# Kernel tuning notes

Measured on AMD Instinct MI355X. Metric: run time of the kernel, lower is better.

## Reference

```python
import jax, jax.numpy as jnp
import numpy as np

B, S, HID = 2, 2048, 2048
NH, NKV, HD = 16, 8, 128
GROUPS = NH // NKV
EPS = 1e-6
SCALING = HD ** -0.5
ROPE_THETA = 1e6


def setup_inputs() -> dict:
    key = jax.random.key(0)
    ks = jax.random.split(key, 8)
    hidden_states = jax.random.normal(ks[0], (B, S, HID), jnp.float32)
    # RoPE tables (Qwen3 style): [B, S, HD]
    pos = jnp.arange(S, dtype=jnp.float32)
    inv_freq = 1.0 / (ROPE_THETA ** (jnp.arange(0, HD, 2, dtype=jnp.float32) / HD))
    ang = pos[:, None] * inv_freq[None, :]            # [S, HD//2]
    emb = jnp.concatenate([ang, ang], axis=-1)        # [S, HD]
    cos = jnp.broadcast_to(jnp.cos(emb)[None], (B, S, HD))
    sin = jnp.broadcast_to(jnp.sin(emb)[None], (B, S, HD))
    # 4D additive causal mask: 0 on/below diagonal, -1e9 above
    causal = jnp.where(jnp.tril(jnp.ones((S, S), bool)), 0.0, -1e9).astype(jnp.float32)
    attention_mask = jnp.broadcast_to(causal[None, None], (B, 1, S, S))
    sc = 0.02
    wq = jax.random.normal(ks[1], (HID, NH * HD), jnp.float32) * sc
    wk = jax.random.normal(ks[2], (HID, NKV * HD), jnp.float32) * sc
    wv = jax.random.normal(ks[3], (HID, NKV * HD), jnp.float32) * sc
    wo = jax.random.normal(ks[4], (NH * HD, HID), jnp.float32) * sc
    q_norm_w = jnp.ones((HD,), jnp.float32)
    k_norm_w = jnp.ones((HD,), jnp.float32)
    return {"hidden_states": hidden_states, "cos": cos, "sin": sin,
            "attention_mask": attention_mask, "wq": wq, "wk": wk, "wv": wv,
            "wo": wo, "q_norm_w": q_norm_w, "k_norm_w": k_norm_w}


def _rmsnorm(x, w, eps=EPS):
    xf = x.astype(jnp.float32)
    var = jnp.mean(xf * xf, axis=-1, keepdims=True)
    return (xf * jax.lax.rsqrt(var + eps)).astype(x.dtype) * w


def _rotate_half(x):
    x1, x2 = x[..., : HD // 2], x[..., HD // 2:]
    return jnp.concatenate([-x2, x1], axis=-1)


def reference(hidden_states, cos, sin, attention_mask, wq, wk, wv, wo, q_norm_w, k_norm_w):
    # projections
    q = jnp.einsum('bsh,hd->bsd', hidden_states, wq).reshape(B, S, NH, HD)
    k = jnp.einsum('bsh,hd->bsd', hidden_states, wk).reshape(B, S, NKV, HD)
    v = jnp.einsum('bsh,hd->bsd', hidden_states, wv).reshape(B, S, NKV, HD)
    # per-head RMSNorm on Q/K (Qwen3RMSNorm over head_dim)
    q = _rmsnorm(q, q_norm_w).transpose(0, 2, 1, 3)   # [B, NH, S, HD]
    k = _rmsnorm(k, k_norm_w).transpose(0, 2, 1, 3)   # [B, NKV, S, HD]
    v = v.transpose(0, 2, 1, 3)                        # [B, NKV, S, HD]
    # RoPE
    c = cos[:, None]  # [B,1,S,HD]
    s = sin[:, None]
    q = q * c + _rotate_half(q) * s
    k = k * c + _rotate_half(k) * s
    # GQA repeat_kv
    k = jnp.repeat(k, GROUPS, axis=1)                  # [B, NH, S, HD]
    v = jnp.repeat(v, GROUPS, axis=1)
    # candidate selection mask: in the source, QK_prune_binary_quant is
    # undefined in this context so the except-branch yields a zero mask -> no-op.
    scores = jnp.einsum('bhqd,bhkd->bhqk', q, k) * SCALING
    scores = scores + attention_mask[:, :, :, :S]      # 4D causal mask branch
    attn_weights = jax.nn.softmax(scores.astype(jnp.float32), axis=-1).astype(q.dtype)
    attn_out = jnp.einsum('bhqk,bhkd->bhqd', attn_weights, v)
    attn_out = attn_out.transpose(0, 2, 1, 3).reshape(B, S, NH * HD)
    attn_out = jnp.einsum('bsd,dh->bsh', attn_out, wo)
    return attn_out, attn_weights
```

## Files before the change

kernel.cpp:

```cpp
#include <hip/hip_runtime.h>
#include <stdint.h>

#define Sn 2048
#define NHn 16
#define NKVn 8
#define HDn 128
#define SCALEf 0.08838834764831845f

using s16x8 = __attribute__((ext_vector_type(8))) short;
using f32x4 = __attribute__((ext_vector_type(4))) float;

__device__ __forceinline__ short f2b(float f) {
  unsigned u = __builtin_bit_cast(unsigned, f);
  u += 0x7fffu + ((u >> 16) & 1u);
  return (short)(u >> 16);
}

__device__ __forceinline__ void gl16(const void* g, void* l) {
  __builtin_amdgcn_global_load_lds((const __attribute__((address_space(1))) void*)g,
                                   (__attribute__((address_space(3))) void*)l, 16, 0, 0);
}

__global__ __launch_bounds__(256) void k_cvt(const float* __restrict__ src, short* __restrict__ dst) {
  int i = blockIdx.x * 256 + threadIdx.x;
  float4 v = ((const float4*)src)[i];
  union { short h[4]; uint2 u; } p;
  p.h[0] = f2b(v.x); p.h[1] = f2b(v.y); p.h[2] = f2b(v.z); p.h[3] = f2b(v.w);
  ((uint2*)dst)[i] = p.u;
}

__global__ __launch_bounds__(256) void k_wt(const float* __restrict__ w, short* __restrict__ wt, int N) {
  __shared__ float t[64][65];
  const int n0 = blockIdx.x * 64, k0 = blockIdx.y * 64;
  const int tid = threadIdx.x;
  const int r = tid >> 2, c0 = (tid & 3) * 16;
  const float* src = w + (size_t)(k0 + r) * N + n0 + c0;
  float4 a = ((const float4*)src)[0];
  float4 b = ((const float4*)src)[1];
  float4 c = ((const float4*)src)[2];
  float4 d = ((const float4*)src)[3];
  float* tr = &t[r][c0];
  tr[0]=a.x; tr[1]=a.y; tr[2]=a.z; tr[3]=a.w;
  tr[4]=b.x; tr[5]=b.y; tr[6]=b.z; tr[7]=b.w;
  tr[8]=c.x; tr[9]=c.y; tr[10]=c.z; tr[11]=c.w;
  tr[12]=d.x; tr[13]=d.y; tr[14]=d.z; tr[15]=d.w;
  __syncthreads();
  union { short h[16]; uint4 u[2]; } p;
#pragma unroll
  for (int j = 0; j < 16; ++j) p.h[j] = f2b(t[c0 + j][r]);
  uint4* dst = (uint4*)(wt + (size_t)(n0 + r) * 2048 + k0 + c0);
  dst[0] = p.u[0]; dst[1] = p.u[1];
}

__global__ __launch_bounds__(256) void k_gemm(const short* __restrict__ A, const short* __restrict__ Bt,
                                              float* __restrict__ C, int M, int N, int K) {
  __shared__ __align__(16) short la[128 * 32];
  __shared__ __align__(16) short lb[128 * 32];
  const int tid = threadIdx.x;
  const int wave = tid >> 6, lane = tid & 63, quad = lane >> 4, lm = lane & 15;
  const int m0 = blockIdx.y * 128, n0 = blockIdx.x * 128;
  const int wm = (wave >> 1) * 64, wn = (wave & 1) * 64;
  const int r0 = tid >> 2, r1 = (256 + tid) >> 2;
  const int q0c = (tid & 3) ^ ((r0 ^ (r0 >> 2)) & 3);
  const int q1c = (tid & 3) ^ ((r1 ^ (r1 >> 2)) & 3);
  const short* gA0 = A + (size_t)(m0 + r0) * K + q0c * 8;
  const short* gA1 = A + (size_t)(m0 + r1) * K + q1c * 8;
  const short* gB0 = Bt + (size_t)(n0 + r0) * K + q0c * 8;
  const short* gB1 = Bt + (size_t)(n0 + r1) * K + q1c * 8;
  short* lA0 = &la[(wave << 6) * 8];
  short* lA1 = &la[(256 + (wave << 6)) * 8];
  short* lB0 = &lb[(wave << 6) * 8];
  short* lB1 = &lb[(256 + (wave << 6)) * 8];
  int aoff[4], boff[4];
#pragma unroll
  for (int mi = 0; mi < 4; ++mi) {
    int r = wm + mi * 16 + lm;
    aoff[mi] = (r * 4 + (quad ^ ((r ^ (r >> 2)) & 3))) * 8;
  }
#pragma unroll
  for (int ni = 0; ni < 4; ++ni) {
    int r = wn + ni * 16 + lm;
    boff[ni] = (r * 4 + (quad ^ ((r ^ (r >> 2)) & 3))) * 8;
  }
  f32x4 acc[4][4] = {};
  for (int k0 = 0; k0 < K; k0 += 32) {
    __syncthreads();
    gl16(gA0 + k0, lA0);
    gl16(gA1 + k0, lA1);
    gl16(gB0 + k0, lB0);
    gl16(gB1 + k0, lB1);
    __syncthreads();
    s16x8 af[4], bfr[4];
#pragma unroll
    for (int mi = 0; mi < 4; ++mi) af[mi] = *(const s16x8*)&la[aoff[mi]];
#pragma unroll
    for (int ni = 0; ni < 4; ++ni) bfr[ni] = *(const s16x8*)&lb[boff[ni]];
#pragma unroll
    for (int mi = 0; mi < 4; ++mi)
#pragma unroll
      for (int ni = 0; ni < 4; ++ni)
        acc[mi][ni] = __builtin_amdgcn_mfma_f32_16x16x32_bf16(af[mi], bfr[ni], acc[mi][ni], 0, 0, 0);
  }
#pragma unroll
  for (int mi = 0; mi < 4; ++mi)
#pragma unroll
    for (int ni = 0; ni < 4; ++ni) {
      size_t base = (size_t)(m0 + wm + mi * 16 + quad * 4) * N + (n0 + wn + ni * 16 + lm);
#pragma unroll
      for (int r = 0; r < 4; ++r)
        C[base + (size_t)r * N] = acc[mi][ni][r];
    }
}

__global__ __launch_bounds__(256) void k_rope(const float* __restrict__ qkv, const float* __restrict__ cosb,
                                              const float* __restrict__ sinb, const float* __restrict__ nw,
                                              short* __restrict__ dst, int nh, int shift, int colbase) {
  const int wid = blockIdx.x * 4 + (threadIdx.x >> 6);
  const int lane = threadIdx.x & 63;
  const int tok = wid >> shift, h = wid & (nh - 1);
  const float* src = qkv + (size_t)tok * 4096 + colbase + h * 128;
  float x0 = src[lane], x1 = src[lane + 64];
  float ss = x0 * x0 + x1 * x1;
#pragma unroll
  for (int off = 32; off > 0; off >>= 1) ss += __shfl_xor(ss, off);
  float rs = rsqrtf(ss * (1.0f / 128.0f) + 1e-6f);
  float xn0 = x0 * rs * nw[lane];
  float xn1 = x1 * rs * nw[lane + 64];
  const float* cb = cosb + (size_t)tok * 128;
  const float* sb = sinb + (size_t)tok * 128;
  float y0 = xn0 * cb[lane] - xn1 * sb[lane];
  float y1 = xn1 * cb[lane + 64] + xn0 * sb[lane + 64];
  int b = tok >> 11, sp = tok & 2047;
  short* d = dst + (((size_t)(b * nh + h)) * 2048 + sp) * 128;
  d[lane] = f2b(y0);
  d[lane + 64] = f2b(y1);
}

__global__ __launch_bounds__(256) void k_vt(const float* __restrict__ qkv, short* __restrict__ VT) {
  __shared__ short t[128 * 66];
  const int tid = threadIdx.x;
  const int s0 = blockIdx.x * 64, hkv = blockIdx.y, b = blockIdx.z;
#pragma unroll
  for (int i = 0; i < 8; ++i) {
    int lin = i * 256 + tid;
    int sl = lin >> 5, d4 = (lin & 31) * 4;
    const float4 v = *(const float4*)(qkv + (size_t)(b * 2048 + s0 + sl) * 4096 + 3072 + hkv * 128 + d4);
    t[(d4 + 0) * 66 + sl] = f2b(v.x);
    t[(d4 + 1) * 66 + sl] = f2b(v.y);
    t[(d4 + 2) * 66 + sl] = f2b(v.z);
    t[(d4 + 3) * 66 + sl] = f2b(v.w);
  }
  __syncthreads();
  const int d = tid >> 1, half = tid & 1;
  union { short h[32]; uint4 u[4]; } p;
#pragma unroll
  for (int j = 0; j < 32; ++j) p.h[j] = t[d * 66 + half * 32 + j];
  uint4* dst = (uint4*)(VT + ((size_t)(b * 8 + hkv) * 128 + d) * 2048 + s0 + half * 32);
  dst[0] = p.u[0]; dst[1] = p.u[1]; dst[2] = p.u[2]; dst[3] = p.u[3];
}

__global__ __launch_bounds__(256) void k_zf(float* __restrict__ W) {
  const int jt = blockIdx.x, it = blockIdx.y, bh = blockIdx.z;
  if (jt <= it) return;
  float* base = W + ((size_t)bh * 2048 + it * 64) * 2048 + jt * 64;
  const float4 z = make_float4(0.f, 0.f, 0.f, 0.f);
#pragma unroll
  for (int i = 0; i < 4; ++i) {
    int lin = i * 256 + threadIdx.x;
    int rr = lin >> 4, c4 = (lin & 15) * 4;
    *(float4*)(base + (size_t)rr * 2048 + c4) = z;
  }
}

__global__ __launch_bounds__(256) void k_attn(const short* __restrict__ Q, const short* __restrict__ Kr,
                                              const short* __restrict__ VT, float* __restrict__ W,
                                              short* __restrict__ OP) {
  __shared__ __align__(16) short qt[64 * 128];
  __shared__ __align__(16) short kt[64 * 128];
  __shared__ __align__(16) short vt[128 * 64];
  __shared__ __align__(16) short pt[64 * 72];
  const int tid = threadIdx.x;
  const int wave = tid >> 6, lane = tid & 63, quad = lane >> 4, lm = lane & 15;
  const int qti = gridDim.x - 1 - blockIdx.x;
  const int h = blockIdx.y, b = blockIdx.z, hkv = h >> 1;
  const int q0 = qti * 64;
  const short* Qb = Q + (((size_t)(b * NHn + h)) * Sn + q0) * HDn;
  const short* Kb = Kr + ((size_t)(b * NKVn + hkv)) * Sn * HDn;
  const short* Vb = VT + ((size_t)(b * NKVn + hkv)) * HDn * Sn;
  float* Wb = W + (((size_t)(b * NHn + h)) * Sn + q0) * (size_t)Sn;

#pragma unroll
  for (int i = 0; i < 4; ++i) {
    int p = i * 256 + tid, r = p >> 4, q = (p & 15) ^ (r & 15);
    gl16(Qb + r * HDn + q * 8, &qt[(i * 256 + (wave << 6)) * 8]);
  }

  float lsum[4] = {0.f, 0.f, 0.f, 0.f};
  for (int jt = 0; jt <= qti; ++jt) {
    const int j0 = jt * 64;
    __syncthreads();
#pragma unroll
    for (int i = 0; i < 4; ++i) {
      int p = i * 256 + tid, r = p >> 4, q = (p & 15) ^ (r & 15);
      gl16(Kb + (size_t)(j0 + r) * HDn + q * 8, &kt[(i * 256 + (wave << 6)) * 8]);
    }
    __syncthreads();
    s16x8 qa[4];
#pragma unroll
    for (int kk = 0; kk < 4; ++kk)
      qa[kk] = *(const s16x8*)&qt[(wave * 16 + lm) * 128 + (((kk * 4 + quad) ^ lm)) * 8];
    f32x4 sa[4] = {};
#pragma unroll
    for (int ni = 0; ni < 4; ++ni)
#pragma unroll
      for (int kk = 0; kk < 4; ++kk) {
        s16x8 kb = *(const s16x8*)&kt[(ni * 16 + lm) * 128 + (((kk * 4 + quad) ^ lm)) * 8];
        sa[ni] = __builtin_amdgcn_mfma_f32_16x16x32_bf16(qa[kk], kb, sa[ni], 0, 0, 0);
      }
    const bool diag = (jt == qti);
#pragma unroll
    for (int ni = 0; ni < 4; ++ni)
#pragma unroll
      for (int r = 0; r < 4; ++r) {
        float e = __expf(sa[ni][r] * SCALEf);
        if (diag && (ni * 16 + lm > wave * 16 + quad * 4 + r)) e = 0.f;
        lsum[r] += e;
      }
  }
  float invl[4];
#pragma unroll
  for (int r = 0; r < 4; ++r) {
    float v = lsum[r];
    v += __shfl_xor(v, 1); v += __shfl_xor(v, 2); v += __shfl_xor(v, 4); v += __shfl_xor(v, 8);
    invl[r] = 1.0f / v;
  }

  f32x4 oa[8] = {};
  for (int jt = 0; jt <= qti; ++jt) {
    const int j0 = jt * 64;
    __syncthreads();
#pragma unroll
    for (int i = 0; i < 4; ++i) {
      int p = i * 256 + tid, r = p >> 4, q = (p & 15) ^ (r & 15);
      gl16(Kb + (size_t)(j0 + r) * HDn + q * 8, &kt[(i * 256 + (wave << 6)) * 8]);
    }
#pragma unroll
    for (int i = 0; i < 4; ++i) {
      int p = i * 256 + tid, r = p >> 3, q = (p & 7) ^ (r & 7);
      gl16(Vb + (size_t)r * Sn + j0 + q * 8, &vt[(i * 256 + (wave << 6)) * 8]);
    }
    __syncthreads();
    s16x8 qa[4];
#pragma unroll
    for (int kk = 0; kk < 4; ++kk)
      qa[kk] = *(const s16x8*)&qt[(wave * 16 + lm) * 128 + (((kk * 4 + quad) ^ lm)) * 8];
    f32x4 sa[4] = {};
#pragma unroll
    for (int ni = 0; ni < 4; ++ni)
#pragma unroll
      for (int kk = 0; kk < 4; ++kk) {
        s16x8 kb = *(const s16x8*)&kt[(ni * 16 + lm) * 128 + (((kk * 4 + quad) ^ lm)) * 8];
        sa[ni] = __builtin_amdgcn_mfma_f32_16x16x32_bf16(qa[kk], kb, sa[ni], 0, 0, 0);
      }
    const bool diag = (jt == qti);
#pragma unroll
    for (int ni = 0; ni < 4; ++ni)
#pragma unroll
      for (int r = 0; r < 4; ++r) {
        float e = __expf(sa[ni][r] * SCALEf) * invl[r];
        if (diag && (ni * 16 + lm > wave * 16 + quad * 4 + r)) e = 0.f;
        Wb[(size_t)(wave * 16 + quad * 4 + r) * Sn + j0 + ni * 16 + lm] = e;
        pt[(wave * 16 + quad * 4 + r) * 72 + ni * 16 + lm] = f2b(e);
      }
    __syncthreads();
    s16x8 pa[2];
#pragma unroll
    for (int kk = 0; kk < 2; ++kk)
      pa[kk] = *(const s16x8*)&pt[(wave * 16 + lm) * 72 + kk * 32 + quad * 8];
#pragma unroll
    for (int ni = 0; ni < 8; ++ni)
#pragma unroll
      for (int kk = 0; kk < 2; ++kk) {
        s16x8 vb = *(const s16x8*)&vt[(ni * 16 + lm) * 64 + (((kk * 4 + quad) ^ (lm & 7))) * 8];
        oa[ni] = __builtin_amdgcn_mfma_f32_16x16x32_bf16(pa[kk], vb, oa[ni], 0, 0, 0);
      }
  }
#pragma unroll
  for (int ni = 0; ni < 8; ++ni)
#pragma unroll
    for (int r = 0; r < 4; ++r)
      OP[(size_t)(b * Sn + q0 + wave * 16 + quad * 4 + r) * 2048 + h * HDn + ni * 16 + lm] = f2b(oa[ni][r]);
}

extern "C" void kernel_launch(void* const* d_in, const int* in_sizes, int n_in,
                              void* d_out, int out_size, void* d_ws, size_t ws_size,
                              hipStream_t stream) {
  const float* hidden = (const float*)d_in[0];
  const float* cosb   = (const float*)d_in[1];
  const float* sinb   = (const float*)d_in[2];
  const float* wq     = (const float*)d_in[4];
  const float* wk     = (const float*)d_in[5];
  const float* wv     = (const float*)d_in[6];
  const float* wo     = (const float*)d_in[7];
  const float* qnw    = (const float*)d_in[8];
  const float* knw    = (const float*)d_in[9];
  float* out  = (float*)d_out;
  float* Wout = out + (size_t)8388608;

  float* qkv   = Wout;
  short* hidB  = (short*)(Wout + (size_t)16777216);
  short* wTall = (short*)(Wout + (size_t)20971520);

  char* wsb = (char*)d_ws;
  short* Qr  = (short*)(wsb);
  short* Kr  = (short*)(wsb + 16777216);
  short* VT  = (short*)(wsb + 25165824);
  short* OP  = (short*)(wsb + 33554432);
  short* woT = (short*)(wsb + 50331648);

  k_cvt<<<8192, 256, 0, stream>>>(hidden, hidB);
  k_wt<<<dim3(32, 32), 256, 0, stream>>>(wq, wTall, 2048);
  k_wt<<<dim3(16, 32), 256, 0, stream>>>(wk, wTall + (size_t)2048 * 2048, 1024);
  k_wt<<<dim3(16, 32), 256, 0, stream>>>(wv, wTall + (size_t)3072 * 2048, 1024);
  k_wt<<<dim3(32, 32), 256, 0, stream>>>(wo, woT, 2048);
  k_gemm<<<dim3(32, 32), 256, 0, stream>>>(hidB, wTall, qkv, 4096, 4096, 2048);
  k_rope<<<16384, 256, 0, stream>>>(qkv, cosb, sinb, qnw, Qr, 16, 4, 0);
  k_rope<<<8192, 256, 0, stream>>>(qkv, cosb, sinb, knw, Kr, 8, 3, 2048);
  k_vt<<<dim3(32, 8, 2), 256, 0, stream>>>(qkv, VT);
  k_zf<<<dim3(32, 32, 32), 256, 0, stream>>>(Wout);
  k_attn<<<dim3(32, 16, 2), 256, 0, stream>>>(Qr, Kr, VT, Wout, OP);
  k_gemm<<<dim3(16, 32), 256, 0, stream>>>(OP, woT, out, 4096, 2048, 2048);
}
```

Measured before the change: 1.010 ms.

## Split attention into single-pass PV kernel and separate tiled weight-writing kernel

The attention kernel now does one pass: it accumulates the unnormalized P·V alongside the row sums (no max subtraction), normalizes at the end, and writes the per-row inverse sums to a workspace. A new fully parallel kernel recomputes QK^T per 64x64 tile, scales by the stored inverse sums, and writes the attention weights (or zeros above the diagonal) with coalesced nontemporal stores through shared memory. This replaces the second pass and the separate zero-fill kernel. The intent is to take the large weight-matrix writes off the imbalanced causal attention critical path and spread them across a big grid, at the cost of recomputing QK^T once more.

```diff
diff --git a/kernel.cpp b/kernel.cpp
--- a/kernel.cpp
+++ b/kernel.cpp
@@ -159,21 +159,8 @@
   dst[0] = p.u[0]; dst[1] = p.u[1]; dst[2] = p.u[2]; dst[3] = p.u[3];
 }
 
-__global__ __launch_bounds__(256) void k_zf(float* __restrict__ W) {
-  const int jt = blockIdx.x, it = blockIdx.y, bh = blockIdx.z;
-  if (jt <= it) return;
-  float* base = W + ((size_t)bh * 2048 + it * 64) * 2048 + jt * 64;
-  const float4 z = make_float4(0.f, 0.f, 0.f, 0.f);
-#pragma unroll
-  for (int i = 0; i < 4; ++i) {
-    int lin = i * 256 + threadIdx.x;
-    int rr = lin >> 4, c4 = (lin & 15) * 4;
-    *(float4*)(base + (size_t)rr * 2048 + c4) = z;
-  }
-}
-
 __global__ __launch_bounds__(256) void k_attn(const short* __restrict__ Q, const short* __restrict__ Kr,
-                                              const short* __restrict__ VT, float* __restrict__ W,
+                                              const short* __restrict__ VT, float* __restrict__ Linv,
                                               short* __restrict__ OP) {
   __shared__ __align__(16) short qt[64 * 128];
   __shared__ __align__(16) short kt[64 * 128];
@@ -187,7 +174,6 @@
   const short* Qb = Q + (((size_t)(b * NHn + h)) * Sn + q0) * HDn;
   const short* Kb = Kr + ((size_t)(b * NKVn + hkv)) * Sn * HDn;
   const short* Vb = VT + ((size_t)(b * NKVn + hkv)) * HDn * Sn;
-  float* Wb = W + (((size_t)(b * NHn + h)) * Sn + q0) * (size_t)Sn;
 
 #pragma unroll
   for (int i = 0; i < 4; ++i) {
@@ -196,6 +182,7 @@
   }
 
   float lsum[4] = {0.f, 0.f, 0.f, 0.f};
+  f32x4 oa[8] = {};
   for (int jt = 0; jt <= qti; ++jt) {
     const int j0 = jt * 64;
     __syncthreads();
@@ -203,6 +190,11 @@
     for (int i = 0; i < 4; ++i) {
       int p = i * 256 + tid, r = p >> 4, q = (p & 15) ^ (r & 15);
       gl16(Kb + (size_t)(j0 + r) * HDn + q * 8, &kt[(i * 256 + (wave << 6)) * 8]);
+    }
+#pragma unroll
+    for (int i = 0; i < 4; ++i) {
+      int p = i * 256 + tid, r = p >> 3, q = (p & 7) ^ (r & 7);
+      gl16(Vb + (size_t)r * Sn + j0 + q * 8, &vt[(i * 256 + (wave << 6)) * 8]);
     }
     __syncthreads();
     s16x8 qa[4];
@@ -225,6 +217,19 @@
         float e = __expf(sa[ni][r] * SCALEf);
         if (diag && (ni * 16 + lm > wave * 16 + quad * 4 + r)) e = 0.f;
         lsum[r] += e;
+        pt[(wave * 16 + quad * 4 + r) * 72 + ni * 16 + lm] = f2b(e);
+      }
+    __syncthreads();
+    s16x8 pa[2];
+#pragma unroll
+    for (int kk = 0; kk < 2; ++kk)
+      pa[kk] = *(const s16x8*)&pt[(wave * 16 + lm) * 72 + kk * 32 + quad * 8];
+#pragma unroll
+    for (int ni = 0; ni < 8; ++ni)
+#pragma unroll
+      for (int kk = 0; kk < 2; ++kk) {
+        s16x8 vb = *(const s16x8*)&vt[(ni * 16 + lm) * 64 + (((kk * 4 + quad) ^ (lm & 7))) * 8];
+        oa[ni] = __builtin_amdgcn_mfma_f32_16x16x32_bf16(pa[kk], vb, oa[ni], 0, 0, 0);
       }
   }
   float invl[4];
@@ -234,62 +239,79 @@
     v += __shfl_xor(v, 1); v += __shfl_xor(v, 2); v += __shfl_xor(v, 4); v += __shfl_xor(v, 8);
     invl[r] = 1.0f / v;
   }
-
-  f32x4 oa[8] = {};
-  for (int jt = 0; jt <= qti; ++jt) {
-    const int j0 = jt * 64;
-    __syncthreads();
+  if (lm == 0) {
+#pragma unroll
+    for (int r = 0; r < 4; ++r)
+      Linv[((size_t)(b * NHn + h)) * Sn + q0 + wave * 16 + quad * 4 + r] = invl[r];
+  }
+#pragma unroll
+  for (int ni = 0; ni < 8; ++ni)
+#pragma unroll
+    for (int r = 0; r < 4; ++r)
+      OP[(size_t)(b * Sn + q0 + wave * 16 + quad * 4 + r) * 2048 + h * HDn + ni * 16 + lm] =
+          f2b(oa[ni][r] * invl[r]);
+}
+
+__global__ __launch_bounds__(256) void k_w(const short* __restrict__ Q, const short* __restrict__ Kr,
+                                           const float* __restrict__ Linv, float* __restrict__ W) {
+  const int jt = blockIdx.x, it = blockIdx.y, bh = blockIdx.z;
+  const int tid = threadIdx.x;
+  float* Wb = W + ((size_t)bh * Sn + (size_t)it * 64) * Sn + jt * 64;
+  if (jt > it) {
+    const f32x4 z = {0.f, 0.f, 0.f, 0.f};
 #pragma unroll
     for (int i = 0; i < 4; ++i) {
-      int p = i * 256 + tid, r = p >> 4, q = (p & 15) ^ (r & 15);
-      gl16(Kb + (size_t)(j0 + r) * HDn + q * 8, &kt[(i * 256 + (wave << 6)) * 8]);
-    }
-#pragma unroll
-    for (int i = 0; i < 4; ++i) {
-      int p = i * 256 + tid, r = p >> 3, q = (p & 7) ^ (r & 7);
-      gl16(Vb + (size_t)r * Sn + j0 + q * 8, &vt[(i * 256 + (wave << 6)) * 8]);
-    }
-    __syncthreads();
-    s16x8 qa[4];
-#pragma unroll
-    for (int kk = 0; kk < 4; ++kk)
-      qa[kk] = *(const s16x8*)&qt[(wave * 16 + lm) * 128 + (((kk * 4 + quad) ^ lm)) * 8];
-    f32x4 sa[4] = {};
-#pragma unroll
-    for (int ni = 0; ni < 4; ++ni)
-#pragma unroll
-      for (int kk = 0; kk < 4; ++kk) {
-        s16x8 kb = *(const s16x8*)&kt[(ni * 16 + lm) * 128 + (((kk * 4 + quad) ^ lm)) * 8];
-        sa[ni] = __builtin_amdgcn_mfma_f32_16x16x32_bf16(qa[kk], kb, sa[ni], 0, 0, 0);
-      }
-    const bool diag = (jt == qti);
-#pragma unroll
-    for (int ni = 0; ni < 4; ++ni)
-#pragma unroll
-      for (int r = 0; r < 4; ++r) {
-        float e = __expf(sa[ni][r] * SCALEf) * invl[r];
-        if (diag && (ni * 16 + lm > wave * 16 + quad * 4 + r)) e = 0.f;
-        Wb[(size_t)(wave * 16 + quad * 4 + r) * Sn + j0 + ni * 16 + lm] = e;
-        pt[(wave * 16 + quad * 4 + r) * 72 + ni * 16 + lm] = f2b(e);
-      }
-    __syncthreads();
-    s16x8 pa[2];
-#pragma unroll
-    for (int kk = 0; kk < 2; ++kk)
-      pa[kk] = *(const s16x8*)&pt[(wave * 16 + lm) * 72 + kk * 32 + quad * 8];
-#pragma unroll
-    for (int ni = 0; ni < 8; ++ni)
-#pragma unroll
-      for (int kk = 0; kk < 2; ++kk) {
-        s16x8 vb = *(const s16x8*)&vt[(ni * 16 + lm) * 64 + (((kk * 4 + quad) ^ (lm & 7))) * 8];
-        oa[ni] = __builtin_amdgcn_mfma_f32_16x16x32_bf16(pa[kk], vb, oa[ni], 0, 0, 0);
-      }
-  }
-#pragma unroll
-  for (int ni = 0; ni < 8; ++ni)
-#pragma unroll
-    for (int r = 0; r < 4; ++r)
-      OP[(size_t)(b * Sn + q0 + wave * 16 + quad * 4 + r) * 2048 + h * HDn + ni * 16 + lm] = f2b(oa[ni][r]);
+      int lin = i * 256 + tid;
+      int rr = lin >> 4, c4 = (lin & 15) * 4;
+      __builtin_nontemporal_store(z, (f32x4*)(Wb + (size_t)rr * Sn + c4));
+    }
+    return;
+  }
+  __shared__ __align__(16) short qt[64 * 128];
+  __shared__ __align__(16) short kt[64 * 128];
+  __shared__ __align__(16) float st[64 * 68];
+  const int wave = tid >> 6, lane = tid & 63, quad = lane >> 4, lm = lane & 15;
+  const int b = bh >> 4, h = bh & 15, hkv = h >> 1;
+  const short* Qb = Q + ((size_t)bh * Sn + (size_t)it * 64) * HDn;
+  const short* Kb = Kr + (((size_t)(b * NKVn + hkv)) * Sn + (size_t)jt * 64) * HDn;
+#pragma unroll
+  for (int i = 0; i < 4; ++i) {
+    int p = i * 256 + tid, r = p >> 4, q = (p & 15) ^ (r & 15);
+    gl16(Qb + r * HDn + q * 8, &qt[(i * 256 + (wave << 6)) * 8]);
+    gl16(Kb + r * HDn + q * 8, &kt[(i * 256 + (wave << 6)) * 8]);
+  }
+  __syncthreads();
+  s16x8 qa[4];
+#pragma unroll
+  for (int kk = 0; kk < 4; ++kk)
+    qa[kk] = *(const s16x8*)&qt[(wave * 16 + lm) * 128 + (((kk * 4 + quad) ^ lm)) * 8];
+  f32x4 sa[4] = {};
+#pragma unroll
+  for (int ni = 0; ni < 4; ++ni)
+#pragma unroll
+    for (int kk = 0; kk < 4; ++kk) {
+      s16x8 kb = *(const s16x8*)&kt[(ni * 16 + lm) * 128 + (((kk * 4 + quad) ^ lm)) * 8];
+      sa[ni] = __builtin_amdgcn_mfma_f32_16x16x32_bf16(qa[kk], kb, sa[ni], 0, 0, 0);
+    }
+  const float* lv = Linv + (size_t)bh * Sn + it * 64;
+  const bool diag = (jt == it);
+#pragma unroll
+  for (int ni = 0; ni < 4; ++ni)
+#pragma unroll
+    for (int r = 0; r < 4; ++r) {
+      int row = wave * 16 + quad * 4 + r, col = ni * 16 + lm;
+      float e = __expf(sa[ni][r] * SCALEf) * lv[row];
+      if (diag && col > row) e = 0.f;
+      st[row * 68 + col] = e;
+    }
+  __syncthreads();
+#pragma unroll
+  for (int i = 0; i < 4; ++i) {
+    int lin = i * 256 + tid;
+    int rr = lin >> 4, c4 = (lin & 15) * 4;
+    f32x4 v = *(const f32x4*)&st[rr * 68 + c4];
+    __builtin_nontemporal_store(v, (f32x4*)(Wb + (size_t)rr * Sn + c4));
+  }
 }
 
 extern "C" void kernel_launch(void* const* d_in, const int* in_sizes, int n_in,
@@ -317,6 +339,7 @@
   short* VT  = (short*)(wsb + 25165824);
   short* OP  = (short*)(wsb + 33554432);
   short* woT = (short*)(wsb + 50331648);
+  float* Linv = (float*)(wsb + 58720256);
 
   k_cvt<<<8192, 256, 0, stream>>>(hidden, hidB);
   k_wt<<<dim3(32, 32), 256, 0, stream>>>(wq, wTall, 2048);
@@ -327,7 +350,7 @@
   k_rope<<<16384, 256, 0, stream>>>(qkv, cosb, sinb, qnw, Qr, 16, 4, 0);
   k_rope<<<8192, 256, 0, stream>>>(qkv, cosb, sinb, knw, Kr, 8, 3, 2048);
   k_vt<<<dim3(32, 8, 2), 256, 0, stream>>>(qkv, VT);
-  k_zf<<<dim3(32, 32, 32), 256, 0, stream>>>(Wout);
-  k_attn<<<dim3(32, 16, 2), 256, 0, stream>>>(Qr, Kr, VT, Wout, OP);
+  k_attn<<<dim3(32, 16, 2), 256, 0, stream>>>(Qr, Kr, VT, Linv, OP);
+  k_w<<<dim3(32, 32, 32), 256, 0, stream>>>(Qr, Kr, Linv, Wout);
   k_gemm<<<dim3(16, 32), 256, 0, stream>>>(OP, woT, out, 4096, 2048, 2048);
 }
```

Result: faster. 945.2 us (-6.4%).
